# Performance work log

Measured on AMD Instinct MI355X. Metric: run time of the kernel, lower is better.

## Reference

```python
import jax, jax.numpy as jnp
import numpy as np

N_NODES = 8192
IN_DIM = 512
H_DIM = 128


def setup_inputs() -> dict:
    key = jax.random.key(0)
    k1, k2, k3, k4 = jax.random.split(key, 4)
    h = jax.random.normal(k1, (N_NODES, IN_DIM), dtype=jnp.float32)
    adj = jax.random.randint(k2, (N_NODES, N_NODES), 0, 2).astype(jnp.float32)
    # xavier-uniform-style scales
    w_scale = float(np.sqrt(6.0 / (IN_DIM + H_DIM)))
    W_w = jax.random.uniform(k3, (H_DIM, IN_DIM), minval=-w_scale, maxval=w_scale, dtype=jnp.float32)
    W_b = jnp.zeros((H_DIM,), dtype=jnp.float32)
    a_scale = float(np.sqrt(6.0 / (1 + H_DIM)))
    a = jax.random.uniform(k4, (1, H_DIM), minval=-a_scale, maxval=a_scale, dtype=jnp.float32)
    return {"h": h, "adj": adj, "W_w": W_w, "W_b": W_b, "a": a}


def reference(h, adj, W_w, W_b, a):
    # Wh: (n, H)
    Wh = h @ W_w.T + W_b
    # (Wh_i + Wh_j) @ a.T == s_i + s_j with s = Wh @ a.T  -> avoids (n,n,H) intermediate
    s = Wh @ a[0]                                  # (n,)
    e = jax.nn.leaky_relu(s[:, None] + s[None, :], negative_slope=0.2)  # (n, n)
    mask = adj != 0
    e = jnp.where(mask, e, -jnp.inf)
    # safe row softmax; rows with no neighbors -> alpha row of zeros (matches nan_to_num)
    m = jnp.max(e, axis=1, keepdims=True)
    m_safe = jnp.where(jnp.isfinite(m), m, 0.0)
    ex = jnp.where(mask, jnp.exp(e - m_safe), 0.0)
    denom = jnp.sum(ex, axis=1, keepdims=True)
    alpha = ex / jnp.where(denom == 0, 1.0, denom)
    z = jax.nn.sigmoid(alpha @ Wh)                 # (n, H)
    return z, alpha
```

## Files before the change

kernel.cpp:

```cpp
#include <hip/hip_runtime.h>
#include <hip/hip_bf16.h>
#include <math.h>

#define N_NODES 8192
#define IN_DIM  512
#define H_DIM   128
#define KC      1024
#define NKB     (N_NODES / KC)
#define BMR     64
#define NTW     (N_NODES / 64)

typedef __attribute__((ext_vector_type(8))) short bf16x8;
typedef __attribute__((ext_vector_type(4))) float f32x4;

__device__ __forceinline__ float lrelu(float x) { return fmaxf(x, 0.2f * x); }

__device__ __forceinline__ unsigned int f2mono(float x) {
    unsigned int b = __float_as_uint(x);
    return (b & 0x80000000u) ? ~b : (b | 0x80000000u);
}
__device__ __forceinline__ float mono2f(unsigned int u) {
    unsigned int b = (u & 0x80000000u) ? (u ^ 0x80000000u) : ~u;
    return __uint_as_float(b);
}

__device__ __forceinline__ short f2bf(float x) {
    union { __hip_bfloat16 h; short s; } cv;
    cv.h = __float2bfloat16(x);
    return cv.s;
}

__global__ __launch_bounds__(256) void k_zero(f32x4* __restrict__ p, int n16) {
    int i = blockIdx.x * 256 + threadIdx.x;
    if (i < n16) {
        f32x4 zv = {0.f, 0.f, 0.f, 0.f};
        __builtin_nontemporal_store(zv, p + i);
    }
}

__global__ __launch_bounds__(256) void k_wh(const float* __restrict__ h,
                                            const float* __restrict__ Ww,
                                            const float* __restrict__ Wb,
                                            float* __restrict__ Wh,
                                            __hip_bfloat16* __restrict__ WhT2) {
    const int BM = 32, BK = 64;
    __shared__ float hT[BK][BM + 4];
    __shared__ float wT[BK][H_DIM + 4];
    const int tid = threadIdx.x;
    const int w = tid >> 6, lane = tid & 63;
    const int trm = tid >> 5, tcm = tid & 31;
    const int row0 = blockIdx.x * BM;

    float acc[4][4] = {};
    for (int k0 = 0; k0 < IN_DIM; k0 += BK) {
        __syncthreads();
        #pragma unroll
        for (int p = 0; p < 8; ++p) {
            int r = 4 * p + w;
            hT[lane][r] = h[(size_t)(row0 + r) * IN_DIM + k0 + lane];
        }
        #pragma unroll
        for (int p = 0; p < 32; ++p) {
            int c = 4 * p + w;
            wT[lane][c] = Ww[(size_t)c * IN_DIM + k0 + lane];
        }
        __syncthreads();
        #pragma unroll 8
        for (int kk = 0; kk < BK; ++kk) {
            f32x4 a4 = *(const f32x4*)&hT[kk][4 * trm];
            f32x4 b4 = *(const f32x4*)&wT[kk][4 * tcm];
            #pragma unroll
            for (int i = 0; i < 4; ++i)
                #pragma unroll
                for (int j = 0; j < 4; ++j)
                    acc[i][j] = fmaf(a4[i], b4[j], acc[i][j]);
        }
    }
    f32x4 wb4 = *(const f32x4*)&Wb[4 * tcm];
    #pragma unroll
    for (int i = 0; i < 4; ++i) {
        int row = row0 + 4 * trm + i;
        f32x4 v;
        #pragma unroll
        for (int jj = 0; jj < 4; ++jj) v[jj] = acc[i][jj] + wb4[jj];
        *(f32x4*)&Wh[(size_t)row * H_DIM + 4 * tcm] = v;
        int ts = row >> 5, kq = (row >> 3) & 3, e = row & 7;
        #pragma unroll
        for (int jj = 0; jj < 4; ++jj) {
            int c = 4 * tcm + jj;
            int f = c >> 4, r16 = c & 15;
            WhT2[((size_t)(ts * 8 + f) * 64 + kq * 16 + r16) * 8 + e] =
                __float2bfloat16(v[jj]);
        }
    }
}

__global__ __launch_bounds__(256) void k_s(const float* __restrict__ Wh,
                                           const float* __restrict__ a,
                                           float* __restrict__ s,
                                           unsigned int* __restrict__ smax) {
    const int w = threadIdx.x >> 6, lane = threadIdx.x & 63;
    const int row = blockIdx.x * 4 + w;
    float2 av = *(const float2*)&a[lane * 2];
    float2 wh = *(const float2*)&Wh[(size_t)row * H_DIM + lane * 2];
    float v = wh.x * av.x + wh.y * av.y;
    #pragma unroll
    for (int off = 32; off > 0; off >>= 1) v += __shfl_down(v, off);
    __shared__ float bmax[4];
    if (lane == 0) { s[row] = v; bmax[w] = v; }
    __syncthreads();
    if (threadIdx.x == 0) {
        float m = fmaxf(fmaxf(bmax[0], bmax[1]), fmaxf(bmax[2], bmax[3]));
        atomicMax(smax, f2mono(m));
    }
}

__global__ __launch_bounds__(256) void k_mask(const float* __restrict__ adj,
                                              unsigned long long* __restrict__ bm) {
    const int lane = threadIdx.x & 63;
    const int row  = blockIdx.x * 4 + (threadIdx.x >> 6);
    const float* arow = adj + (size_t)row * N_NODES;
    unsigned long long* mrow = bm + (size_t)row * NTW;
    #pragma unroll 4
    for (int c = 0; c < N_NODES / 256; ++c) {
        f32x4 a4 = __builtin_nontemporal_load((const f32x4*)(arow + c * 256 + lane * 4));
        unsigned long long v = 0ull;
        v |= (a4[0] != 0.f) ? 1ull : 0ull;
        v |= (a4[1] != 0.f) ? 2ull : 0ull;
        v |= (a4[2] != 0.f) ? 4ull : 0ull;
        v |= (a4[3] != 0.f) ? 8ull : 0ull;
        v <<= (4 * (lane & 15));
        v |= __shfl_xor(v, 1);
        v |= __shfl_xor(v, 2);
        v |= __shfl_xor(v, 4);
        v |= __shfl_xor(v, 8);
        if ((lane & 15) == 0)
            mrow[c * 4 + (lane >> 4)] = v;
    }
}

__global__ __launch_bounds__(256) void k_A(const unsigned long long* __restrict__ bm,
                                           const __hip_bfloat16* __restrict__ WhT2,
                                           const float* __restrict__ s,
                                           const unsigned int* __restrict__ smaxp,
                                           float* __restrict__ denom,
                                           float* __restrict__ y) {
    const int lane = threadIdx.x & 63;
    const int w    = threadIdx.x >> 6;
    const int r16  = lane & 15;
    const int kq   = lane >> 4;
    const int row0 = blockIdx.x * BMR;
    const int j0   = blockIdx.y * KC;
    const int rowA = row0 + w * 16 + r16;

    const float smax = mono2f(*smaxp);
    const float si = s[rowA];
    const float mi = lrelu(si + smax);

    f32x4 acc[8] = {{0.f,0.f,0.f,0.f},{0.f,0.f,0.f,0.f},{0.f,0.f,0.f,0.f},{0.f,0.f,0.f,0.f},
                    {0.f,0.f,0.f,0.f},{0.f,0.f,0.f,0.f},{0.f,0.f,0.f,0.f},{0.f,0.f,0.f,0.f}};
    float dsum = 0.f;

    const float* sp = s + j0 + kq * 8;
    const unsigned long long* mrow = bm + (size_t)rowA * NTW + (j0 >> 6);

    for (int bs = 0; bs < KC / 64; ++bs) {
        unsigned long long m64 = mrow[bs];
        #pragma unroll
        for (int sub = 0; sub < 2; ++sub) {
            const int ts = bs * 2 + sub;
            unsigned int bits = (unsigned int)(m64 >> (sub * 32 + kq * 8)) & 0xffu;

            f32x4 sc0 = *(const f32x4*)(sp + ts * 32);
            f32x4 sc1 = *(const f32x4*)(sp + ts * 32 + 4);
            float sv[8] = {sc0[0], sc0[1], sc0[2], sc0[3], sc1[0], sc1[1], sc1[2], sc1[3]};
            bf16x8 afrag;
            #pragma unroll
            for (int e = 0; e < 8; ++e) {
                bool nb = (bits >> e) & 1u;
                float ex = nb ? __expf(lrelu(si + sv[e]) - mi) : 0.f;
                dsum += ex;
                afrag[e] = f2bf(ex);
            }
            const __hip_bfloat16* base =
                WhT2 + (size_t)((j0 >> 5) + ts) * 4096 + lane * 8;
            #pragma unroll
            for (int half = 0; half < 2; ++half) {
                bf16x8 bc[4];
                #pragma unroll
                for (int f = 0; f < 4; ++f)
                    bc[f] = *(const bf16x8*)(base + (half * 4 + f) * 512);
                #pragma unroll
                for (int f = 0; f < 4; ++f)
                    acc[half * 4 + f] =
                        __builtin_amdgcn_mfma_f32_16x16x32_bf16(afrag, bc[f], acc[half * 4 + f], 0, 0, 0);
            }
        }
    }

    {
        float v = dsum;
        v += __shfl_xor(v, 16);
        v += __shfl_xor(v, 32);
        if (lane < 16) atomicAdd(&denom[row0 + w * 16 + lane], v);
    }
    #pragma unroll
    for (int f = 0; f < 8; ++f)
        #pragma unroll
        for (int i = 0; i < 4; ++i) {
            int rr = row0 + w * 16 + kq * 4 + i;
            int cc = f * 16 + r16;
            atomicAdd(&y[(size_t)rr * H_DIM + cc], acc[f][i]);
        }
}

__global__ __launch_bounds__(256) void k_A_fb(const float* __restrict__ adj,
                                              const __hip_bfloat16* __restrict__ WhT2,
                                              const float* __restrict__ s,
                                              const unsigned int* __restrict__ smaxp,
                                              float* __restrict__ denom,
                                              float* __restrict__ y) {
    __shared__ unsigned char msk[BMR * 64];
    const int tid  = threadIdx.x;
    const int lane = tid & 63;
    const int w    = tid >> 6;
    const int r16  = lane & 15;
    const int kq   = lane >> 4;
    const int row0 = blockIdx.x * BMR;
    const int j0base = blockIdx.y * KC;
    const int rowA = row0 + w * 16 + r16;

    const float smax = mono2f(*smaxp);
    const float si = s[rowA];
    const float mi = lrelu(si + smax);

    f32x4 acc[8] = {{0.f,0.f,0.f,0.f},{0.f,0.f,0.f,0.f},{0.f,0.f,0.f,0.f},{0.f,0.f,0.f,0.f},
                    {0.f,0.f,0.f,0.f},{0.f,0.f,0.f,0.f},{0.f,0.f,0.f,0.f},{0.f,0.f,0.f,0.f}};
    float dsum = 0.f;

    const float* sp = s + j0base + kq * 8;

    int sRow[4], sCol[4];
    #pragma unroll
    for (int p = 0; p < 4; ++p) {
        int seg = p * 256 + tid;
        sRow[p] = seg >> 4;
        sCol[p] = (seg & 15) * 4;
    }
    const int NBIG = KC / 64;
    f32x4 areg[4];
    #pragma unroll
    for (int p = 0; p < 4; ++p)
        areg[p] = __builtin_nontemporal_load(
            (const f32x4*)(adj + (size_t)(row0 + sRow[p]) * N_NODES + j0base + sCol[p]));

    for (int bs = 0; bs < NBIG; ++bs) {
        __syncthreads();
        #pragma unroll
        for (int p = 0; p < 4; ++p) {
            f32x4 a4 = areg[p];
            unsigned int mwd = 0u;
            mwd |= (a4[0] != 0.f) ? 0x00000001u : 0u;
            mwd |= (a4[1] != 0.f) ? 0x00000100u : 0u;
            mwd |= (a4[2] != 0.f) ? 0x00010000u : 0u;
            mwd |= (a4[3] != 0.f) ? 0x01000000u : 0u;
            int r = sRow[p], c = sCol[p];
            int slot = (c >> 3) ^ (r & 7);
            *(unsigned int*)&msk[r * 64 + (slot << 3) + (c & 7)] = mwd;
        }
        __syncthreads();
        if (bs + 1 < NBIG) {
            const int j1 = j0base + (bs + 1) * 64;
            #pragma unroll
            for (int p = 0; p < 4; ++p)
                areg[p] = __builtin_nontemporal_load(
                    (const f32x4*)(adj + (size_t)(row0 + sRow[p]) * N_NODES + j1 + sCol[p]));
        }
        #pragma unroll
        for (int sub = 0; sub < 2; ++sub) {
            const int ts = bs * 2 + sub;
            const int rT = w * 16 + r16;
            const int slotR = (sub * 4 + kq) ^ (r16 & 7);
            unsigned long long m8 = *(const unsigned long long*)&msk[rT * 64 + (slotR << 3)];
            unsigned int bits = (unsigned int)((m8 * 0x0102040810204080ull) >> 56) & 0xffu;

            f32x4 sc0 = *(const f32x4*)(sp + ts * 32);
            f32x4 sc1 = *(const f32x4*)(sp + ts * 32 + 4);
            float sv[8] = {sc0[0], sc0[1], sc0[2], sc0[3], sc1[0], sc1[1], sc1[2], sc1[3]};
            bf16x8 afrag;
            #pragma unroll
            for (int e = 0; e < 8; ++e) {
                bool nb = (bits >> e) & 1u;
                float ex = nb ? __expf(lrelu(si + sv[e]) - mi) : 0.f;
                dsum += ex;
                afrag[e] = f2bf(ex);
            }
            const __hip_bfloat16* base =
                WhT2 + (size_t)((j0base >> 5) + ts) * 4096 + lane * 8;
            #pragma unroll
            for (int half = 0; half < 2; ++half) {
                bf16x8 bc[4];
                #pragma unroll
                for (int f = 0; f < 4; ++f)
                    bc[f] = *(const bf16x8*)(base + (half * 4 + f) * 512);
                #pragma unroll
                for (int f = 0; f < 4; ++f)
                    acc[half * 4 + f] =
                        __builtin_amdgcn_mfma_f32_16x16x32_bf16(afrag, bc[f], acc[half * 4 + f], 0, 0, 0);
            }
        }
    }
    {
        float v = dsum;
        v += __shfl_xor(v, 16);
        v += __shfl_xor(v, 32);
        if (lane < 16) atomicAdd(&denom[row0 + w * 16 + lane], v);
    }
    #pragma unroll
    for (int f = 0; f < 8; ++f)
        #pragma unroll
        for (int i = 0; i < 4; ++i) {
            int rr = row0 + w * 16 + kq * 4 + i;
            int cc = f * 16 + r16;
            atomicAdd(&y[(size_t)rr * H_DIM + cc], acc[f][i]);
        }
}

__global__ __launch_bounds__(256) void k_B(const unsigned long long* __restrict__ bmask,
                                           const float* __restrict__ adj,
                                           const float* __restrict__ s,
                                           const float* __restrict__ denom,
                                           const unsigned int* __restrict__ smaxp,
                                           float* __restrict__ alpha,
                                           int use_mask) {
    const int NSTEP = N_NODES / 256;
    const int w = threadIdx.x >> 6, lane = threadIdx.x & 63;
    const int row = blockIdx.x * 4 + w;
    const float smax = mono2f(*smaxp);
    const float si = s[row];
    const float mi = lrelu(si + smax);
    const float d = denom[row];
    const float rd = d > 0.f ? 1.f / d : 0.f;
    float* arow = alpha + (size_t)row * N_NODES;
    if (use_mask) {
        const unsigned long long* mrow = bmask + (size_t)row * NTW;
        #pragma unroll 4
        for (int t = 0; t < NSTEP; ++t) {
            int col = t * 256 + lane * 4;
            unsigned long long mb = mrow[t * 4 + (lane >> 4)];
            int sh = (lane & 15) * 4;
            f32x4 sj = *(const f32x4*)&s[col];
            f32x4 o;
            o[0] = ((mb >> (sh + 0)) & 1ull) ? __expf(lrelu(si + sj[0]) - mi) * rd : 0.f;
            o[1] = ((mb >> (sh + 1)) & 1ull) ? __expf(lrelu(si + sj[1]) - mi) * rd : 0.f;
            o[2] = ((mb >> (sh + 2)) & 1ull) ? __expf(lrelu(si + sj[2]) - mi) * rd : 0.f;
            o[3] = ((mb >> (sh + 3)) & 1ull) ? __expf(lrelu(si + sj[3]) - mi) * rd : 0.f;
            __builtin_nontemporal_store(o, (f32x4*)&arow[col]);
        }
    } else {
        const float* adjrow = adj + (size_t)row * N_NODES;
        #pragma unroll 4
        for (int t = 0; t < NSTEP; ++t) {
            int col = t * 256 + lane * 4;
            f32x4 a4 = __builtin_nontemporal_load((const f32x4*)&adjrow[col]);
            f32x4 sj = *(const f32x4*)&s[col];
            f32x4 o;
            o[0] = (a4[0] != 0.f) ? __expf(lrelu(si + sj[0]) - mi) * rd : 0.f;
            o[1] = (a4[1] != 0.f) ? __expf(lrelu(si + sj[1]) - mi) * rd : 0.f;
            o[2] = (a4[2] != 0.f) ? __expf(lrelu(si + sj[2]) - mi) * rd : 0.f;
            o[3] = (a4[3] != 0.f) ? __expf(lrelu(si + sj[3]) - mi) * rd : 0.f;
            __builtin_nontemporal_store(o, (f32x4*)&arow[col]);
        }
    }
}

__global__ __launch_bounds__(256) void k_z(const float* __restrict__ y,
                                           const float* __restrict__ denom,
                                           float* __restrict__ z) {
    int i = blockIdx.x * 256 + threadIdx.x;
    int row = i >> 7;
    float d = denom[row];
    float rd = d > 0.f ? 1.f / d : 0.f;
    float v = y[i] * rd;
    z[i] = 1.f / (1.f + __expf(-v));
}

extern "C" void kernel_launch(void* const* d_in, const int* in_sizes, int n_in,
                              void* d_out, int out_size, void* d_ws, size_t ws_size,
                              hipStream_t stream) {
    const float* h   = (const float*)d_in[0];
    const float* adj = (const float*)d_in[1];
    const float* Ww  = (const float*)d_in[2];
    const float* Wb  = (const float*)d_in[3];
    const float* a   = (const float*)d_in[4];

    float* z     = (float*)d_out;
    float* alpha = z + (size_t)N_NODES * H_DIM;

    char* ws = (char*)d_ws;
    float* y     = (float*)ws;  ws += sizeof(float) * (size_t)N_NODES * H_DIM;
    float* denom = (float*)ws;  ws += sizeof(float) * N_NODES;
    unsigned int* smax = (unsigned int*)ws;  ws += 256;
    size_t zero_bytes = (size_t)(ws - (char*)d_ws);
    float* Wh    = (float*)ws;  ws += sizeof(float) * (size_t)N_NODES * H_DIM;
    __hip_bfloat16* WhT2 = (__hip_bfloat16*)ws;
    ws += sizeof(__hip_bfloat16) * (size_t)N_NODES * H_DIM;
    float* s     = (float*)ws;  ws += sizeof(float) * N_NODES;
    unsigned long long* bmask = (unsigned long long*)ws;
    size_t base_need  = (size_t)(ws - (char*)d_ws);
    size_t mask_bytes = (size_t)N_NODES * NTW * sizeof(unsigned long long);
    int use_mask = (ws_size >= base_need + mask_bytes) ? 1 : 0;

    int n16 = (int)(zero_bytes / 16);
    hipLaunchKernelGGL(k_zero, dim3((n16 + 255) / 256), dim3(256), 0, stream,
                       (f32x4*)d_ws, n16);
    if (use_mask)
        hipLaunchKernelGGL(k_mask, dim3(N_NODES / 4), dim3(256), 0, stream, adj, bmask);
    hipLaunchKernelGGL(k_wh, dim3(N_NODES / 32), dim3(256), 0, stream, h, Ww, Wb, Wh, WhT2);
    hipLaunchKernelGGL(k_s,  dim3(N_NODES / 4),  dim3(256), 0, stream, Wh, a, s, smax);
    if (use_mask)
        hipLaunchKernelGGL(k_A, dim3(N_NODES / BMR, NKB), dim3(256), 0, stream,
                           bmask, WhT2, s, smax, denom, y);
    else
        hipLaunchKernelGGL(k_A_fb, dim3(N_NODES / BMR, NKB), dim3(256), 0, stream,
                           adj, WhT2, s, smax, denom, y);
    hipLaunchKernelGGL(k_B,  dim3(N_NODES / 4),  dim3(256), 0, stream,
                       bmask, adj, s, denom, smax, alpha, use_mask);
    hipLaunchKernelGGL(k_z,  dim3((N_NODES * H_DIM) / 256), dim3(256), 0, stream,
                       y, denom, z);
}
```

Baseline: 252.4 us.

## Process two row tiles per wave in k_A and replace y atomics with partials

Each wave in k_A now computes 32 rows instead of 16, so every B-fragment load from WhT2 feeds two MFMAs and the block tile grows to 128 rows. The float atomicAdd into y is replaced by plain stores into per-K-chunk partial buffers, and a new k_z2 kernel sums the 8 partials before the sigmoid. This removes atomic contention and halves global reads of WhT2. The cost is more accumulator registers (possibly lower occupancy), about 32MB of extra workspace traffic, and half as many blocks in the grid.

New measurement: 244.5 us. -3.1%, faster.

```diff
diff --git a/kernel.cpp b/kernel.cpp
--- a/kernel.cpp
+++ b/kernel.cpp
@@ -7,7 +7,7 @@
 #define H_DIM   128
 #define KC      1024
 #define NKB     (N_NODES / KC)
-#define BMR     64
+#define BMRA    128
 #define NTW     (N_NODES / 64)
 
 typedef __attribute__((ext_vector_type(8))) short bf16x8;
@@ -144,43 +144,54 @@
                                            const float* __restrict__ s,
                                            const unsigned int* __restrict__ smaxp,
                                            float* __restrict__ denom,
-                                           float* __restrict__ y) {
+                                           float* __restrict__ y,
+                                           float* __restrict__ ypart,
+                                           int use_part) {
     const int lane = threadIdx.x & 63;
     const int w    = threadIdx.x >> 6;
     const int r16  = lane & 15;
     const int kq   = lane >> 4;
-    const int row0 = blockIdx.x * BMR;
+    const int rowB = blockIdx.x * BMRA + w * 32;
     const int j0   = blockIdx.y * KC;
-    const int rowA = row0 + w * 16 + r16;
+    const int rowA0 = rowB + r16;
+    const int rowA1 = rowB + 16 + r16;
 
     const float smax = mono2f(*smaxp);
-    const float si = s[rowA];
-    const float mi = lrelu(si + smax);
-
-    f32x4 acc[8] = {{0.f,0.f,0.f,0.f},{0.f,0.f,0.f,0.f},{0.f,0.f,0.f,0.f},{0.f,0.f,0.f,0.f},
-                    {0.f,0.f,0.f,0.f},{0.f,0.f,0.f,0.f},{0.f,0.f,0.f,0.f},{0.f,0.f,0.f,0.f}};
-    float dsum = 0.f;
+    const float si0 = s[rowA0], si1 = s[rowA1];
+    const float mi0 = lrelu(si0 + smax), mi1 = lrelu(si1 + smax);
+
+    f32x4 acc0[8], acc1[8];
+    {
+        f32x4 zv = {0.f, 0.f, 0.f, 0.f};
+        #pragma unroll
+        for (int f = 0; f < 8; ++f) { acc0[f] = zv; acc1[f] = zv; }
+    }
+    float dsum0 = 0.f, dsum1 = 0.f;
 
     const float* sp = s + j0 + kq * 8;
-    const unsigned long long* mrow = bm + (size_t)rowA * NTW + (j0 >> 6);
+    const unsigned long long* mrow0 = bm + (size_t)rowA0 * NTW + (j0 >> 6);
+    const unsigned long long* mrow1 = bm + (size_t)rowA1 * NTW + (j0 >> 6);
 
     for (int bs = 0; bs < KC / 64; ++bs) {
-        unsigned long long m64 = mrow[bs];
+        unsigned long long m64a = mrow0[bs];
+        unsigned long long m64b = mrow1[bs];
         #pragma unroll
         for (int sub = 0; sub < 2; ++sub) {
             const int ts = bs * 2 + sub;
-            unsigned int bits = (unsigned int)(m64 >> (sub * 32 + kq * 8)) & 0xffu;
+            unsigned int bits0 = (unsigned int)(m64a >> (sub * 32 + kq * 8)) & 0xffu;
+            unsigned int bits1 = (unsigned int)(m64b >> (sub * 32 + kq * 8)) & 0xffu;
 
             f32x4 sc0 = *(const f32x4*)(sp + ts * 32);
             f32x4 sc1 = *(const f32x4*)(sp + ts * 32 + 4);
             float sv[8] = {sc0[0], sc0[1], sc0[2], sc0[3], sc1[0], sc1[1], sc1[2], sc1[3]};
-            bf16x8 afrag;
+            bf16x8 af0, af1;
             #pragma unroll
             for (int e = 0; e < 8; ++e) {
-                bool nb = (bits >> e) & 1u;
-                float ex = nb ? __expf(lrelu(si + sv[e]) - mi) : 0.f;
-                dsum += ex;
-                afrag[e] = f2bf(ex);
+                float ex0 = ((bits0 >> e) & 1u) ? __expf(lrelu(si0 + sv[e]) - mi0) : 0.f;
+                float ex1 = ((bits1 >> e) & 1u) ? __expf(lrelu(si1 + sv[e]) - mi1) : 0.f;
+                dsum0 += ex0; dsum1 += ex1;
+                af0[e] = f2bf(ex0);
+                af1[e] = f2bf(ex1);
             }
             const __hip_bfloat16* base =
                 WhT2 + (size_t)((j0 >> 5) + ts) * 4096 + lane * 8;
@@ -191,27 +202,45 @@
                 for (int f = 0; f < 4; ++f)
                     bc[f] = *(const bf16x8*)(base + (half * 4 + f) * 512);
                 #pragma unroll
-                for (int f = 0; f < 4; ++f)
-                    acc[half * 4 + f] =
-                        __builtin_amdgcn_mfma_f32_16x16x32_bf16(afrag, bc[f], acc[half * 4 + f], 0, 0, 0);
+                for (int f = 0; f < 4; ++f) {
+                    acc0[half * 4 + f] =
+                        __builtin_amdgcn_mfma_f32_16x16x32_bf16(af0, bc[f], acc0[half * 4 + f], 0, 0, 0);
+                    acc1[half * 4 + f] =
+                        __builtin_amdgcn_mfma_f32_16x16x32_bf16(af1, bc[f], acc1[half * 4 + f], 0, 0, 0);
+                }
             }
         }
     }
 
     {
-        float v = dsum;
-        v += __shfl_xor(v, 16);
-        v += __shfl_xor(v, 32);
-        if (lane < 16) atomicAdd(&denom[row0 + w * 16 + lane], v);
-    }
-    #pragma unroll
-    for (int f = 0; f < 8; ++f)
-        #pragma unroll
-        for (int i = 0; i < 4; ++i) {
-            int rr = row0 + w * 16 + kq * 4 + i;
-            int cc = f * 16 + r16;
-            atomicAdd(&y[(size_t)rr * H_DIM + cc], acc[f][i]);
-        }
+        float v0 = dsum0, v1 = dsum1;
+        v0 += __shfl_xor(v0, 16); v0 += __shfl_xor(v0, 32);
+        v1 += __shfl_xor(v1, 16); v1 += __shfl_xor(v1, 32);
+        if (lane < 16) {
+            atomicAdd(&denom[rowB + lane], v0);
+            atomicAdd(&denom[rowB + 16 + lane], v1);
+        }
+    }
+    if (use_part) {
+        float* yp = ypart + (size_t)blockIdx.y * N_NODES * H_DIM;
+        #pragma unroll
+        for (int f = 0; f < 8; ++f)
+            #pragma unroll
+            for (int i = 0; i < 4; ++i) {
+                int cc = f * 16 + r16;
+                yp[(size_t)(rowB + kq * 4 + i) * H_DIM + cc] = acc0[f][i];
+                yp[(size_t)(rowB + 16 + kq * 4 + i) * H_DIM + cc] = acc1[f][i];
+            }
+    } else {
+        #pragma unroll
+        for (int f = 0; f < 8; ++f)
+            #pragma unroll
+            for (int i = 0; i < 4; ++i) {
+                int cc = f * 16 + r16;
+                atomicAdd(&y[(size_t)(rowB + kq * 4 + i) * H_DIM + cc], acc0[f][i]);
+                atomicAdd(&y[(size_t)(rowB + 16 + kq * 4 + i) * H_DIM + cc], acc1[f][i]);
+            }
+    }
 }
 
 __global__ __launch_bounds__(256) void k_A_fb(const float* __restrict__ adj,
@@ -220,13 +249,13 @@
                                               const unsigned int* __restrict__ smaxp,
                                               float* __restrict__ denom,
                                               float* __restrict__ y) {
-    __shared__ unsigned char msk[BMR * 64];
+    __shared__ unsigned char msk[64 * 64];
     const int tid  = threadIdx.x;
     const int lane = tid & 63;
     const int w    = tid >> 6;
     const int r16  = lane & 15;
     const int kq   = lane >> 4;
-    const int row0 = blockIdx.x * BMR;
+    const int row0 = blockIdx.x * 64;
     const int j0base = blockIdx.y * KC;
     const int rowA = row0 + w * 16 + r16;
 
@@ -234,8 +263,12 @@
     const float si = s[rowA];
     const float mi = lrelu(si + smax);
 
-    f32x4 acc[8] = {{0.f,0.f,0.f,0.f},{0.f,0.f,0.f,0.f},{0.f,0.f,0.f,0.f},{0.f,0.f,0.f,0.f},
-                    {0.f,0.f,0.f,0.f},{0.f,0.f,0.f,0.f},{0.f,0.f,0.f,0.f},{0.f,0.f,0.f,0.f}};
+    f32x4 acc[8];
+    {
+        f32x4 zv = {0.f, 0.f, 0.f, 0.f};
+        #pragma unroll
+        for (int f = 0; f < 8; ++f) acc[f] = zv;
+    }
     float dsum = 0.f;
 
     const float* sp = s + j0base + kq * 8;
@@ -385,6 +418,21 @@
     z[i] = 1.f / (1.f + __expf(-v));
 }
 
+__global__ __launch_bounds__(256) void k_z2(const float* __restrict__ ypart,
+                                            const float* __restrict__ denom,
+                                            float* __restrict__ z) {
+    int i = blockIdx.x * 256 + threadIdx.x;
+    int row = i >> 7;
+    float d = denom[row];
+    float rd = d > 0.f ? 1.f / d : 0.f;
+    float v = 0.f;
+    #pragma unroll
+    for (int p = 0; p < NKB; ++p)
+        v += ypart[(size_t)p * N_NODES * H_DIM + i];
+    v *= rd;
+    z[i] = 1.f / (1.f + __expf(-v));
+}
+
 extern "C" void kernel_launch(void* const* d_in, const int* in_sizes, int n_in,
                               void* d_out, int out_size, void* d_ws, size_t ws_size,
                               hipStream_t stream) {
@@ -407,9 +455,13 @@
     ws += sizeof(__hip_bfloat16) * (size_t)N_NODES * H_DIM;
     float* s     = (float*)ws;  ws += sizeof(float) * N_NODES;
     unsigned long long* bmask = (unsigned long long*)ws;
-    size_t base_need  = (size_t)(ws - (char*)d_ws);
-    size_t mask_bytes = (size_t)N_NODES * NTW * sizeof(unsigned long long);
-    int use_mask = (ws_size >= base_need + mask_bytes) ? 1 : 0;
+    ws += (size_t)N_NODES * NTW * sizeof(unsigned long long);
+    size_t mask_need = (size_t)(ws - (char*)d_ws);
+    float* ypart = (float*)ws;
+    ws += (size_t)NKB * N_NODES * H_DIM * sizeof(float);
+    size_t part_need = (size_t)(ws - (char*)d_ws);
+    int use_mask = (ws_size >= mask_need) ? 1 : 0;
+    int use_part = (use_mask && ws_size >= part_need) ? 1 : 0;
 
     int n16 = (int)(zero_bytes / 16);
     hipLaunchKernelGGL(k_zero, dim3((n16 + 255) / 256), dim3(256), 0, stream,
@@ -419,13 +471,17 @@
     hipLaunchKernelGGL(k_wh, dim3(N_NODES / 32), dim3(256), 0, stream, h, Ww, Wb, Wh, WhT2);
     hipLaunchKernelGGL(k_s,  dim3(N_NODES / 4),  dim3(256), 0, stream, Wh, a, s, smax);
     if (use_mask)
-        hipLaunchKernelGGL(k_A, dim3(N_NODES / BMR, NKB), dim3(256), 0, stream,
-                           bmask, WhT2, s, smax, denom, y);
+        hipLaunchKernelGGL(k_A, dim3(N_NODES / BMRA, NKB), dim3(256), 0, stream,
+                           bmask, WhT2, s, smax, denom, y, ypart, use_part);
     else
-        hipLaunchKernelGGL(k_A_fb, dim3(N_NODES / BMR, NKB), dim3(256), 0, stream,
+        hipLaunchKernelGGL(k_A_fb, dim3(N_NODES / 64, NKB), dim3(256), 0, stream,
                            adj, WhT2, s, smax, denom, y);
     hipLaunchKernelGGL(k_B,  dim3(N_NODES / 4),  dim3(256), 0, stream,
                        bmask, adj, s, denom, smax, alpha, use_mask);
-    hipLaunchKernelGGL(k_z,  dim3((N_NODES * H_DIM) / 256), dim3(256), 0, stream,
-                       y, denom, z);
-}
+    if (use_part)
+        hipLaunchKernelGGL(k_z2, dim3((N_NODES * H_DIM) / 256), dim3(256), 0, stream,
+                           ypart, denom, z);
+    else
+        hipLaunchKernelGGL(k_z, dim3((N_NODES * H_DIM) / 256), dim3(256), 0, stream,
+                           y, denom, z);
+}
```
